# Kernel tuning notes

Hardware: AMD Instinct MI355X
Metric: run time of the kernel (lower is better)

Reference implementation:

```python
import jax, jax.numpy as jnp
import numpy as np

# dims: batch B, frames F_, spatial tokens N, heads H, head dim D, model dim DIM
B, F_, N, H, D, DIM = 1, 16, 1024, 8, 64, 512


def setup_inputs() -> dict:
    key = jax.random.key(0)
    k1, k2, k3, k4 = jax.random.split(key, 4)
    x = jax.random.normal(k1, (B, F_ * N, DIM), dtype=jnp.float32)
    W_qkv = jax.random.normal(k2, (DIM, 3 * H * D), dtype=jnp.float32) * 0.02
    W_out = jax.random.normal(k3, (H * D, DIM), dtype=jnp.float32) * 0.02
    mask = jax.random.randint(k4, (1, 1, N), 0, 2, dtype=jnp.int32)
    return {"x": x, "W_qkv": W_qkv, "W_out": W_out, "mask": mask, "diag": 1}


def reference(x, W_qkv, W_out, mask, diag):
    scale = D ** -0.5
    qkv = x @ W_qkv                      # [B, F*N, 3*H*D]
    q, k, v = jnp.split(qkv, 3, axis=-1)

    def split_heads(t):                  # 'b n (h d) -> (b h) n d'
        return t.reshape(B, F_ * N, H, D).transpose(0, 2, 1, 3).reshape(B * H, F_ * N, D)

    q, k, v = map(split_heads, (q, k, v))
    q = q * scale

    def axial(t):                        # '(b h) (f n) d -> (b h f) n d'
        return t.reshape(B * H * F_, N, D)

    q, k, v = map(axial, (q, k, v))

    sim = jnp.einsum('bid,bjd->bij', q, k)        # [(B*H*F), N, N]
    neg = -jnp.finfo(sim.dtype).max
    if diag:
        sim = jnp.where(jnp.eye(N, dtype=bool)[None], neg, sim)
    sim = jnp.where(mask == 0, neg, sim)           # padding mask broadcast
    attn = jax.nn.softmax(sim, axis=-1)
    out = jnp.einsum('bij,bjd->bid', attn, v)      # [(B*H*F), N, D]

    # '(b h f) n d -> (b h) (f n) d' then '(b h) n d -> b n (h d)'
    out = out.reshape(B, H, F_ * N, D).transpose(0, 2, 1, 3).reshape(B, F_ * N, H * D)
    return out @ W_out
```

## Files before the change

kernel.cpp:

```cpp
#include <hip/hip_runtime.h>
#include <stdint.h>

typedef __bf16 bf16;
typedef __bf16 bf16x8 __attribute__((ext_vector_type(8)));
typedef float f32x4 __attribute__((ext_vector_type(4)));

__device__ __forceinline__ void gload_lds16(const void* g, void* l) {
    __builtin_amdgcn_global_load_lds((const __attribute__((address_space(1))) void*)g,
                                     (__attribute__((address_space(3))) void*)l, 16, 0, 0);
}

__device__ __forceinline__ float fast_exp2(float x) { return __builtin_amdgcn_exp2f(x); }

__global__ __launch_bounds__(256) void k_cvt(const float* __restrict__ x, bf16* __restrict__ xb, int n8) {
    int i = blockIdx.x * 256 + threadIdx.x;
    if (i >= n8) return;
    const f32x4* p = (const f32x4*)(x + (size_t)i * 8);
    f32x4 a = p[0], b = p[1];
    bf16x8 o;
    o[0] = (bf16)a[0]; o[1] = (bf16)a[1]; o[2] = (bf16)a[2]; o[3] = (bf16)a[3];
    o[4] = (bf16)b[0]; o[5] = (bf16)b[1]; o[6] = (bf16)b[2]; o[7] = (bf16)b[3];
    *(bf16x8*)(xb + (size_t)i * 8) = o;
}

__global__ __launch_bounds__(256) void k_tx(const float* __restrict__ W, bf16* __restrict__ WT, int R, int C) {
    __shared__ float t[32][33];
    int n0 = blockIdx.x * 32, k0 = blockIdx.y * 32;
    int tx = threadIdx.x, ty = threadIdx.y;
    for (int i = 0; i < 32; i += 8) t[ty + i][tx] = W[(size_t)(k0 + ty + i) * C + n0 + tx];
    __syncthreads();
    for (int i = 0; i < 32; i += 8) WT[(size_t)(n0 + ty + i) * R + k0 + tx] = (bf16)t[tx][ty + i];
}

__global__ __launch_bounds__(256) void k_scan(const int* __restrict__ mask, int* __restrict__ idxU,
                                              int* __restrict__ cpos, int* __restrict__ meta) {
    __shared__ int lsum[256];
    int t = threadIdx.x;
    int m[4], s = 0;
#pragma unroll
    for (int e = 0; e < 4; e++) { m[e] = mask[4 * t + e]; s += m[e]; }
    lsum[t] = s;
    __syncthreads();
    for (int off = 1; off < 256; off <<= 1) {
        int v = (t >= off) ? lsum[t - off] : 0;
        __syncthreads();
        lsum[t] += v;
        __syncthreads();
    }
    int run = lsum[t] - s;
#pragma unroll
    for (int e = 0; e < 4; e++) {
        if (m[e]) { idxU[run] = 4 * t + e; cpos[4 * t + e] = run; run++; }
        else cpos[4 * t + e] = -1;
    }
    if (t == 255) { meta[0] = lsum[255]; meta[1] = (lsum[255] + 63) >> 6; }
}

__global__ __launch_bounds__(256) void k_zpad(bf16* __restrict__ Kc, const int* __restrict__ meta) {
    int bp = blockIdx.x;
    int nU = meta[0], nUp = meta[1] << 6;
    int n = (nUp - nU) * 64;
    for (int idx = threadIdx.x; idx < n; idx += 256) {
        int r = nU + (idx >> 6), d = idx & 63;
        Kc[((size_t)bp * 1024 + r) * 64 + d] = (bf16)0.f;
    }
}

__global__ __launch_bounds__(512) void k_qkv(const bf16* __restrict__ Xb, const bf16* __restrict__ WT,
                                             bf16* __restrict__ Qb, bf16* __restrict__ Kc,
                                             bf16* __restrict__ Vc, const int* __restrict__ cpos) {
    __shared__ char As[32768], Bs[16384];
    int tid = threadIdx.x, l = tid & 63, w = tid >> 6;
    int wy = w & 3, wx = w >> 2;
    int id = blockIdx.x;
    int wg = (id & 7) * 96 + (id >> 3);
    int bm = (wg / 12) * 256, bn = (wg % 12) * 128;
    int lr = l & 15, kg = l >> 4;
    int rsub = tid >> 3;
    int csrc = (tid & 7) ^ (rsub & 7);
    f32x4 acc[4][4] = {};

    for (int k0 = 0; k0 < 512; k0 += 64) {
        __syncthreads();
#pragma unroll
        for (int i = 0; i < 4; i++)
            gload_lds16((const char*)Xb + ((size_t)(bm + i * 64 + rsub) * 512 + k0) * 2 + csrc * 16,
                        As + i * 8192 + tid * 16);
#pragma unroll
        for (int i = 0; i < 2; i++)
            gload_lds16((const char*)WT + ((size_t)(bn + i * 64 + rsub) * 512 + k0) * 2 + csrc * 16,
                        Bs + i * 8192 + tid * 16);
        __syncthreads();
#pragma unroll
        for (int kk = 0; kk < 2; kk++) {
            int sb = kk * 4 + kg;
            bf16x8 af[4], bfr[4];
#pragma unroll
            for (int mt = 0; mt < 4; mt++) {
                int r = wy * 64 + mt * 16 + lr;
                af[mt] = *(const bf16x8*)(As + r * 128 + ((sb ^ (r & 7)) << 4));
            }
#pragma unroll
            for (int nt = 0; nt < 4; nt++) {
                int r = wx * 64 + nt * 16 + lr;
                bfr[nt] = *(const bf16x8*)(Bs + r * 128 + ((sb ^ (r & 7)) << 4));
            }
#pragma unroll
            for (int mt = 0; mt < 4; mt++)
#pragma unroll
                for (int nt = 0; nt < 4; nt++)
                    acc[mt][nt] = __builtin_amdgcn_mfma_f32_16x16x32_bf16(af[mt], bfr[nt], acc[mt][nt], 0, 0, 0);
        }
    }

    int cb = bn + wx * 64;
    int which = cb >> 9, hd = cb & 511, h = hd >> 6;
#pragma unroll
    for (int mt = 0; mt < 4; mt++) {
#pragma unroll
        for (int j = 0; j < 4; j++) {
            int m = bm + wy * 64 + mt * 16 + kg * 4 + j;
            int f = m >> 10, nn = m & 1023;
            int bpb = h * 16 + f;
            if (which == 0) {
#pragma unroll
                for (int nt = 0; nt < 4; nt++)
                    Qb[((size_t)bpb * 1024 + nn) * 64 + nt * 16 + lr] = (bf16)(acc[mt][nt][j] * 0.18033688f);
            } else {
                int cr = cpos[nn];
                if (cr >= 0) {
                    bf16* base = (which == 1) ? Kc : Vc;
#pragma unroll
                    for (int nt = 0; nt < 4; nt++)
                        base[((size_t)bpb * 1024 + cr) * 64 + nt * 16 + lr] = (bf16)acc[mt][nt][j];
                }
            }
        }
    }
}

__global__ __launch_bounds__(256) void k_vtg(const bf16* __restrict__ Vc, bf16* __restrict__ Vtc,
                                             const int* __restrict__ meta) {
    __shared__ bf16 t[64][80];
    int bp = blockIdx.y, c0 = blockIdx.x * 64;
    int nU = meta[0], nUp = meta[1] << 6;
    if (c0 >= nUp) return;
    int tid = threadIdx.x;
    int nl = tid >> 2, dc = (tid & 3) * 16;
    int c = c0 + nl;
    bf16x8 a0 = {}, a1 = {};
    if (c < nU) {
        const bf16* src = Vc + ((size_t)bp * 1024 + c) * 64 + dc;
        a0 = *(const bf16x8*)src;
        a1 = *(const bf16x8*)(src + 8);
    }
    *(bf16x8*)&t[nl][dc] = a0;
    *(bf16x8*)&t[nl][dc + 8] = a1;
    __syncthreads();
    int dl = tid >> 2, nc = (tid & 3) * 16;
    bf16x8 o0, o1;
#pragma unroll
    for (int i = 0; i < 8; i++) o0[i] = t[nc + i][dl];
#pragma unroll
    for (int i = 0; i < 8; i++) o1[i] = t[nc + 8 + i][dl];
    bf16* dst = Vtc + ((size_t)bp * 64 + dl) * 1024 + c0 + nc;
    *(bf16x8*)dst = o0;
    *(bf16x8*)(dst + 8) = o1;
}

__global__ __launch_bounds__(512) void k_attn(const bf16* __restrict__ Qb, const bf16* __restrict__ Kc,
                                              const bf16* __restrict__ Vtc, bf16* __restrict__ AO,
                                              const int* __restrict__ cpos, const int* __restrict__ meta,
                                              const int* __restrict__ diagp) {
    __shared__ char Ks[8192], Vs[8192], Ps[16384];
    int tid = threadIdx.x, l = tid & 63, w = tid >> 6;
    int id = blockIdx.x;
    int wg = (id & 7) * 128 + (id >> 3);
    int qt = wg & 7, bp = wg >> 3;
    int lr = l & 15, kg = l >> 4;
    int diag = diagp[0];
    int nU = meta[0], nT = meta[1];

    int nq = qt * 128 + w * 16 + lr;
    const char* Qrow = (const char*)Qb + ((size_t)bp * 1024 + nq) * 128;
    bf16x8 qf0 = *(const bf16x8*)(Qrow + kg * 16);
    bf16x8 qf1 = *(const bf16x8*)(Qrow + 64 + kg * 16);

    int cq[4];
#pragma unroll
    for (int j = 0; j < 4; j++) {
        int qg = qt * 128 + w * 16 + kg * 4 + j;
        cq[j] = diag ? cpos[qg] : -1;
    }

    const char* Kbase = (const char*)Kc + (size_t)bp * 1024 * 128;
    const char* Vbase = (const char*)Vtc + (size_t)bp * 64 * 2048;

    int rs = tid >> 3;
    int cs = (tid & 7) ^ (rs & 7);

    f32x4 o[4] = {};
    f32x4 psum = {0.f, 0.f, 0.f, 0.f};

    for (int kt = 0; kt < nT; kt++) {
        __syncthreads();
        gload_lds16(Kbase + (size_t)(kt * 64 + rs) * 128 + cs * 16, Ks + w * 1024);
        gload_lds16(Vbase + (size_t)rs * 2048 + kt * 128 + cs * 16, Vs + w * 1024);
        __syncthreads();

        f32x4 s[4] = {};
#pragma unroll
        for (int nt = 0; nt < 4; nt++) {
            int r = nt * 16 + lr;
            bf16x8 kf0 = *(const bf16x8*)(Ks + r * 128 + ((kg ^ (r & 7)) << 4));
            bf16x8 kf1 = *(const bf16x8*)(Ks + r * 128 + (((4 + kg) ^ (r & 7)) << 4));
            s[nt] = __builtin_amdgcn_mfma_f32_16x16x32_bf16(qf0, kf0, s[nt], 0, 0, 0);
            s[nt] = __builtin_amdgcn_mfma_f32_16x16x32_bf16(qf1, kf1, s[nt], 0, 0, 0);
        }

        float mf0 = (kt * 64 + lr < nU) ? 1.f : 0.f;
        float mf1 = (kt * 64 + 16 + lr < nU) ? 1.f : 0.f;
        float mf2 = (kt * 64 + 32 + lr < nU) ? 1.f : 0.f;
        float mf3 = (kt * 64 + 48 + lr < nU) ? 1.f : 0.f;
#pragma unroll
        for (int j = 0; j < 4; j++) {
            s[0][j] = fast_exp2(s[0][j]) * mf0;
            s[1][j] = fast_exp2(s[1][j]) * mf1;
            s[2][j] = fast_exp2(s[2][j]) * mf2;
            s[3][j] = fast_exp2(s[3][j]) * mf3;
        }
#pragma unroll
        for (int nt = 0; nt < 4; nt++) {
            int c = kt * 64 + nt * 16 + lr;
#pragma unroll
            for (int j = 0; j < 4; j++)
                if (c == cq[j]) s[nt][j] = 0.f;
        }
#pragma unroll
        for (int j = 0; j < 4; j++) psum[j] += (s[0][j] + s[1][j]) + (s[2][j] + s[3][j]);

#pragma unroll
        for (int nt = 0; nt < 4; nt++)
#pragma unroll
            for (int j = 0; j < 4; j++) {
                int rq = w * 16 + kg * 4 + j;
                int byte = (rq * 128 + (nt * 16 + lr) * 2) ^ ((rq & 7) << 4);
                *(bf16*)(Ps + byte) = (bf16)s[nt][j];
            }

        int rp = w * 16 + lr;
        bf16x8 pf0 = *(const bf16x8*)(Ps + rp * 128 + ((kg ^ (rp & 7)) << 4));
        bf16x8 pf1 = *(const bf16x8*)(Ps + rp * 128 + (((4 + kg) ^ (rp & 7)) << 4));
#pragma unroll
        for (int dt = 0; dt < 4; dt++) {
            int rd = dt * 16 + lr;
            bf16x8 vf0 = *(const bf16x8*)(Vs + rd * 128 + ((kg ^ (rd & 7)) << 4));
            bf16x8 vf1 = *(const bf16x8*)(Vs + rd * 128 + (((4 + kg) ^ (rd & 7)) << 4));
            o[dt] = __builtin_amdgcn_mfma_f32_16x16x32_bf16(pf0, vf0, o[dt], 0, 0, 0);
            o[dt] = __builtin_amdgcn_mfma_f32_16x16x32_bf16(pf1, vf1, o[dt], 0, 0, 0);
        }
    }

#pragma unroll
    for (int off = 1; off < 16; off <<= 1)
#pragma unroll
        for (int j = 0; j < 4; j++) psum[j] += __shfl_xor(psum[j], off, 64);
    float inv[4];
#pragma unroll
    for (int j = 0; j < 4; j++) inv[j] = 1.0f / psum[j];

    int f = bp & 15, h = bp >> 4;
#pragma unroll
    for (int dt = 0; dt < 4; dt++)
#pragma unroll
        for (int j = 0; j < 4; j++) {
            int n = qt * 128 + w * 16 + kg * 4 + j;
            size_t m = (size_t)f * 1024 + n;
            AO[m * 512 + h * 64 + dt * 16 + lr] = (bf16)(o[dt][j] * inv[j]);
        }
}

__global__ __launch_bounds__(256) void k_out(const bf16* __restrict__ Ab, const bf16* __restrict__ WT,
                                             float* __restrict__ out) {
    __shared__ char As[16384], Bs[16384];
    int tid = threadIdx.x, l = tid & 63, w = tid >> 6;
    int wy = w >> 1, wx = w & 1;
    int id = blockIdx.x;
    int wg = (id & 7) * 64 + (id >> 3);
    int bm = (wg / 4) * 128, bn = (wg % 4) * 128;
    int lr = l & 15, kg = l >> 4;
    int p = l & 7, rsub = l >> 3;
    int csrc = p ^ rsub;
    f32x4 acc[4][4] = {};

    for (int k0 = 0; k0 < 512; k0 += 64) {
        __syncthreads();
#pragma unroll
        for (int i = 0; i < 4; i++) {
            int rt = w * 32 + i * 8 + rsub;
            gload_lds16((const char*)Ab + ((size_t)(bm + rt) * 512 + k0) * 2 + csrc * 16,
                        As + w * 4096 + i * 1024 + l * 16);
            gload_lds16((const char*)WT + ((size_t)(bn + rt) * 512 + k0) * 2 + csrc * 16,
                        Bs + w * 4096 + i * 1024 + l * 16);
        }
        __syncthreads();
#pragma unroll
        for (int kk = 0; kk < 2; kk++) {
            bf16x8 af[4], bfr[4];
            int sb = (kk * 4 + kg);
#pragma unroll
            for (int mt = 0; mt < 4; mt++) {
                int r = wy * 64 + mt * 16 + lr;
                af[mt] = *(const bf16x8*)(As + r * 128 + ((sb ^ (lr & 7)) << 4));
            }
#pragma unroll
            for (int nt = 0; nt < 4; nt++) {
                int r = wx * 64 + nt * 16 + lr;
                bfr[nt] = *(const bf16x8*)(Bs + r * 128 + ((sb ^ (lr & 7)) << 4));
            }
#pragma unroll
            for (int mt = 0; mt < 4; mt++)
#pragma unroll
                for (int nt = 0; nt < 4; nt++)
                    acc[mt][nt] = __builtin_amdgcn_mfma_f32_16x16x32_bf16(af[mt], bfr[nt], acc[mt][nt], 0, 0, 0);
        }
    }
#pragma unroll
    for (int mt = 0; mt < 4; mt++)
#pragma unroll
        for (int nt = 0; nt < 4; nt++) {
            int c = bn + wx * 64 + nt * 16 + lr;
#pragma unroll
            for (int j = 0; j < 4; j++) {
                int m = bm + wy * 64 + mt * 16 + kg * 4 + j;
                out[(size_t)m * 512 + c] = acc[mt][nt][j];
            }
        }
}

extern "C" void kernel_launch(void* const* d_in, const int* in_sizes, int n_in,
                              void* d_out, int out_size, void* d_ws, size_t ws_size,
                              hipStream_t stream) {
    const float* x    = (const float*)d_in[0];
    const float* Wqkv = (const float*)d_in[1];
    const float* Wout = (const float*)d_in[2];
    const int*   mask = (const int*)d_in[3];
    const int*   diag = (const int*)d_in[4];
    float* out = (float*)d_out;
    char* ws = (char*)d_ws;

    bf16* Xb  = (bf16*)(ws);
    bf16* AO  = (bf16*)(ws);
    bf16* WqT = (bf16*)(ws + ((size_t)16 << 20));
    bf16* WoT = (bf16*)(ws + ((size_t)18 << 20));
    int*  idxU = (int*)(ws + ((size_t)18 << 20) + (1 << 19));
    int*  cpos = (int*)(ws + ((size_t)18 << 20) + (1 << 19) + 4096);
    int*  meta = (int*)(ws + ((size_t)18 << 20) + (1 << 19) + 8192);
    bf16* Qb  = (bf16*)(ws + ((size_t)19 << 20));
    bf16* Kc  = (bf16*)(ws + ((size_t)35 << 20));
    bf16* Vc  = (bf16*)(ws + ((size_t)51 << 20));
    bf16* Vtc = (bf16*)(ws + ((size_t)67 << 20));

    hipLaunchKernelGGL(k_cvt, dim3(4096), dim3(256), 0, stream, x, Xb, 1048576);
    hipLaunchKernelGGL(k_tx,  dim3(48, 16), dim3(32, 8), 0, stream, Wqkv, WqT, 512, 1536);
    hipLaunchKernelGGL(k_tx,  dim3(16, 16), dim3(32, 8), 0, stream, Wout, WoT, 512, 512);
    hipLaunchKernelGGL(k_scan, dim3(1), dim3(256), 0, stream, mask, idxU, cpos, meta);
    hipLaunchKernelGGL(k_zpad, dim3(128), dim3(256), 0, stream, Kc, meta);
    hipLaunchKernelGGL(k_qkv, dim3(768), dim3(512), 0, stream, Xb, WqT, Qb, Kc, Vc, cpos);
    hipLaunchKernelGGL(k_vtg, dim3(16, 128), dim3(256), 0, stream, Vc, Vtc, meta);
    hipLaunchKernelGGL(k_attn, dim3(1024), dim3(512), 0, stream, Qb, Kc, Vtc, AO, cpos, meta, diag);
    hipLaunchKernelGGL(k_out, dim3(512), dim3(256), 0, stream, AO, WoT, out);
}
```

Measured before the change: 123.0 us.

## Shrink QKV GEMM tile to 128x128 and load two KV tiles per attention sync

The QKV projection kernel goes from 512-thread blocks with 256x128 tiles to 256-thread blocks with 128x128 tiles. The grid doubles to 1536 blocks, LDS per block shrinks, and the load swizzle is rewritten per wave. The attention kernel now double-buffers K/V in LDS, loading two 64-key tiles between one pair of barriers so the barrier count per key is halved. This trades more LDS per attention block, and possibly lower occupancy, for fewer synchronisations, and trades A-tile reuse in the GEMM for more parallel blocks.

```diff
diff --git a/kernel.cpp b/kernel.cpp
--- a/kernel.cpp
+++ b/kernel.cpp
@@ -66,44 +66,44 @@
     }
 }
 
-__global__ __launch_bounds__(512) void k_qkv(const bf16* __restrict__ Xb, const bf16* __restrict__ WT,
+__global__ __launch_bounds__(256) void k_qkv(const bf16* __restrict__ Xb, const bf16* __restrict__ WT,
                                              bf16* __restrict__ Qb, bf16* __restrict__ Kc,
                                              bf16* __restrict__ Vc, const int* __restrict__ cpos) {
-    __shared__ char As[32768], Bs[16384];
+    __shared__ char As[16384], Bs[16384];
     int tid = threadIdx.x, l = tid & 63, w = tid >> 6;
-    int wy = w & 3, wx = w >> 2;
+    int wy = w >> 1, wx = w & 1;
     int id = blockIdx.x;
-    int wg = (id & 7) * 96 + (id >> 3);
-    int bm = (wg / 12) * 256, bn = (wg % 12) * 128;
+    int wg = (id & 7) * 192 + (id >> 3);
+    int bm = (wg / 12) * 128, bn = (wg % 12) * 128;
     int lr = l & 15, kg = l >> 4;
-    int rsub = tid >> 3;
-    int csrc = (tid & 7) ^ (rsub & 7);
+    int p = l & 7, rsub = l >> 3;
+    int csrc = p ^ rsub;
     f32x4 acc[4][4] = {};
 
     for (int k0 = 0; k0 < 512; k0 += 64) {
         __syncthreads();
 #pragma unroll
-        for (int i = 0; i < 4; i++)
-            gload_lds16((const char*)Xb + ((size_t)(bm + i * 64 + rsub) * 512 + k0) * 2 + csrc * 16,
-                        As + i * 8192 + tid * 16);
-#pragma unroll
-        for (int i = 0; i < 2; i++)
-            gload_lds16((const char*)WT + ((size_t)(bn + i * 64 + rsub) * 512 + k0) * 2 + csrc * 16,
-                        Bs + i * 8192 + tid * 16);
+        for (int i = 0; i < 4; i++) {
+            int rt = w * 32 + i * 8 + rsub;
+            gload_lds16((const char*)Xb + ((size_t)(bm + rt) * 512 + k0) * 2 + csrc * 16,
+                        As + w * 4096 + i * 1024 + l * 16);
+            gload_lds16((const char*)WT + ((size_t)(bn + rt) * 512 + k0) * 2 + csrc * 16,
+                        Bs + w * 4096 + i * 1024 + l * 16);
+        }
         __syncthreads();
 #pragma unroll
         for (int kk = 0; kk < 2; kk++) {
-            int sb = kk * 4 + kg;
             bf16x8 af[4], bfr[4];
+            int sb = (kk * 4 + kg);
 #pragma unroll
             for (int mt = 0; mt < 4; mt++) {
                 int r = wy * 64 + mt * 16 + lr;
-                af[mt] = *(const bf16x8*)(As + r * 128 + ((sb ^ (r & 7)) << 4));
+                af[mt] = *(const bf16x8*)(As + r * 128 + ((sb ^ (lr & 7)) << 4));
             }
 #pragma unroll
             for (int nt = 0; nt < 4; nt++) {
                 int r = wx * 64 + nt * 16 + lr;
-                bfr[nt] = *(const bf16x8*)(Bs + r * 128 + ((sb ^ (r & 7)) << 4));
+                bfr[nt] = *(const bf16x8*)(Bs + r * 128 + ((sb ^ (lr & 7)) << 4));
             }
 #pragma unroll
             for (int mt = 0; mt < 4; mt++)
@@ -172,7 +172,7 @@
                                               const bf16* __restrict__ Vtc, bf16* __restrict__ AO,
                                               const int* __restrict__ cpos, const int* __restrict__ meta,
                                               const int* __restrict__ diagp) {
-    __shared__ char Ks[8192], Vs[8192], Ps[16384];
+    __shared__ char Ks[2][8192], Vs[2][8192], Ps[16384];
     int tid = threadIdx.x, l = tid & 63, w = tid >> 6;
     int id = blockIdx.x;
     int wg = (id & 7) * 128 + (id >> 3);
@@ -180,6 +180,7 @@
     int lr = l & 15, kg = l >> 4;
     int diag = diagp[0];
     int nU = meta[0], nT = meta[1];
+    int nT2 = (nT + 1) >> 1;
 
     int nq = qt * 128 + w * 16 + lr;
     const char* Qrow = (const char*)Qb + ((size_t)bp * 1024 + nq) * 128;
@@ -202,62 +203,74 @@
     f32x4 o[4] = {};
     f32x4 psum = {0.f, 0.f, 0.f, 0.f};
 
-    for (int kt = 0; kt < nT; kt++) {
-        __syncthreads();
-        gload_lds16(Kbase + (size_t)(kt * 64 + rs) * 128 + cs * 16, Ks + w * 1024);
-        gload_lds16(Vbase + (size_t)rs * 2048 + kt * 128 + cs * 16, Vs + w * 1024);
-        __syncthreads();
-
-        f32x4 s[4] = {};
-#pragma unroll
-        for (int nt = 0; nt < 4; nt++) {
-            int r = nt * 16 + lr;
-            bf16x8 kf0 = *(const bf16x8*)(Ks + r * 128 + ((kg ^ (r & 7)) << 4));
-            bf16x8 kf1 = *(const bf16x8*)(Ks + r * 128 + (((4 + kg) ^ (r & 7)) << 4));
-            s[nt] = __builtin_amdgcn_mfma_f32_16x16x32_bf16(qf0, kf0, s[nt], 0, 0, 0);
-            s[nt] = __builtin_amdgcn_mfma_f32_16x16x32_bf16(qf1, kf1, s[nt], 0, 0, 0);
-        }
-
-        float mf0 = (kt * 64 + lr < nU) ? 1.f : 0.f;
-        float mf1 = (kt * 64 + 16 + lr < nU) ? 1.f : 0.f;
-        float mf2 = (kt * 64 + 32 + lr < nU) ? 1.f : 0.f;
-        float mf3 = (kt * 64 + 48 + lr < nU) ? 1.f : 0.f;
-#pragma unroll
-        for (int j = 0; j < 4; j++) {
-            s[0][j] = fast_exp2(s[0][j]) * mf0;
-            s[1][j] = fast_exp2(s[1][j]) * mf1;
-            s[2][j] = fast_exp2(s[2][j]) * mf2;
-            s[3][j] = fast_exp2(s[3][j]) * mf3;
-        }
-#pragma unroll
-        for (int nt = 0; nt < 4; nt++) {
-            int c = kt * 64 + nt * 16 + lr;
-#pragma unroll
-            for (int j = 0; j < 4; j++)
-                if (c == cq[j]) s[nt][j] = 0.f;
-        }
-#pragma unroll
-        for (int j = 0; j < 4; j++) psum[j] += (s[0][j] + s[1][j]) + (s[2][j] + s[3][j]);
-
-#pragma unroll
-        for (int nt = 0; nt < 4; nt++)
+    for (int kt2 = 0; kt2 < nT2; kt2++) {
+        int ktA = kt2 * 2;
+        int nH = (ktA + 1 < nT) ? 2 : 1;
+        __syncthreads();
+        gload_lds16(Kbase + (size_t)(ktA * 64 + rs) * 128 + cs * 16, Ks[0] + w * 1024);
+        gload_lds16(Vbase + (size_t)rs * 2048 + ktA * 128 + cs * 16, Vs[0] + w * 1024);
+        if (nH == 2) {
+            gload_lds16(Kbase + (size_t)((ktA + 1) * 64 + rs) * 128 + cs * 16, Ks[1] + w * 1024);
+            gload_lds16(Vbase + (size_t)rs * 2048 + (ktA + 1) * 128 + cs * 16, Vs[1] + w * 1024);
+        }
+        __syncthreads();
+
+        for (int hh = 0; hh < nH; hh++) {
+            int kt = ktA + hh;
+            const char* Kt = Ks[hh];
+            const char* Vt = Vs[hh];
+
+            f32x4 s[4] = {};
+#pragma unroll
+            for (int nt = 0; nt < 4; nt++) {
+                int r = nt * 16 + lr;
+                bf16x8 kf0 = *(const bf16x8*)(Kt + r * 128 + ((kg ^ (r & 7)) << 4));
+                bf16x8 kf1 = *(const bf16x8*)(Kt + r * 128 + (((4 + kg) ^ (r & 7)) << 4));
+                s[nt] = __builtin_amdgcn_mfma_f32_16x16x32_bf16(qf0, kf0, s[nt], 0, 0, 0);
+                s[nt] = __builtin_amdgcn_mfma_f32_16x16x32_bf16(qf1, kf1, s[nt], 0, 0, 0);
+            }
+
+            float mf0 = (kt * 64 + lr < nU) ? 1.f : 0.f;
+            float mf1 = (kt * 64 + 16 + lr < nU) ? 1.f : 0.f;
+            float mf2 = (kt * 64 + 32 + lr < nU) ? 1.f : 0.f;
+            float mf3 = (kt * 64 + 48 + lr < nU) ? 1.f : 0.f;
 #pragma unroll
             for (int j = 0; j < 4; j++) {
-                int rq = w * 16 + kg * 4 + j;
-                int byte = (rq * 128 + (nt * 16 + lr) * 2) ^ ((rq & 7) << 4);
-                *(bf16*)(Ps + byte) = (bf16)s[nt][j];
-            }
-
-        int rp = w * 16 + lr;
-        bf16x8 pf0 = *(const bf16x8*)(Ps + rp * 128 + ((kg ^ (rp & 7)) << 4));
-        bf16x8 pf1 = *(const bf16x8*)(Ps + rp * 128 + (((4 + kg) ^ (rp & 7)) << 4));
-#pragma unroll
-        for (int dt = 0; dt < 4; dt++) {
-            int rd = dt * 16 + lr;
-            bf16x8 vf0 = *(const bf16x8*)(Vs + rd * 128 + ((kg ^ (rd & 7)) << 4));
-            bf16x8 vf1 = *(const bf16x8*)(Vs + rd * 128 + (((4 + kg) ^ (rd & 7)) << 4));
-            o[dt] = __builtin_amdgcn_mfma_f32_16x16x32_bf16(pf0, vf0, o[dt], 0, 0, 0);
-            o[dt] = __builtin_amdgcn_mfma_f32_16x16x32_bf16(pf1, vf1, o[dt], 0, 0, 0);
+                s[0][j] = fast_exp2(s[0][j]) * mf0;
+                s[1][j] = fast_exp2(s[1][j]) * mf1;
+                s[2][j] = fast_exp2(s[2][j]) * mf2;
+                s[3][j] = fast_exp2(s[3][j]) * mf3;
+            }
+#pragma unroll
+            for (int nt = 0; nt < 4; nt++) {
+                int c = kt * 64 + nt * 16 + lr;
+#pragma unroll
+                for (int j = 0; j < 4; j++)
+                    if (c == cq[j]) s[nt][j] = 0.f;
+            }
+#pragma unroll
+            for (int j = 0; j < 4; j++) psum[j] += (s[0][j] + s[1][j]) + (s[2][j] + s[3][j]);
+
+#pragma unroll
+            for (int nt = 0; nt < 4; nt++)
+#pragma unroll
+                for (int j = 0; j < 4; j++) {
+                    int rq = w * 16 + kg * 4 + j;
+                    int byte = (rq * 128 + (nt * 16 + lr) * 2) ^ ((rq & 7) << 4);
+                    *(bf16*)(Ps + byte) = (bf16)s[nt][j];
+                }
+
+            int rp = w * 16 + lr;
+            bf16x8 pf0 = *(const bf16x8*)(Ps + rp * 128 + ((kg ^ (rp & 7)) << 4));
+            bf16x8 pf1 = *(const bf16x8*)(Ps + rp * 128 + (((4 + kg) ^ (rp & 7)) << 4));
+#pragma unroll
+            for (int dt = 0; dt < 4; dt++) {
+                int rd = dt * 16 + lr;
+                bf16x8 vf0 = *(const bf16x8*)(Vt + rd * 128 + ((kg ^ (rd & 7)) << 4));
+                bf16x8 vf1 = *(const bf16x8*)(Vt + rd * 128 + (((4 + kg) ^ (rd & 7)) << 4));
+                o[dt] = __builtin_amdgcn_mfma_f32_16x16x32_bf16(pf0, vf0, o[dt], 0, 0, 0);
+                o[dt] = __builtin_amdgcn_mfma_f32_16x16x32_bf16(pf1, vf1, o[dt], 0, 0, 0);
+            }
         }
     }
 
@@ -366,7 +379,7 @@
     hipLaunchKernelGGL(k_tx,  dim3(16, 16), dim3(32, 8), 0, stream, Wout, WoT, 512, 512);
     hipLaunchKernelGGL(k_scan, dim3(1), dim3(256), 0, stream, mask, idxU, cpos, meta);
     hipLaunchKernelGGL(k_zpad, dim3(128), dim3(256), 0, stream, Kc, meta);
-    hipLaunchKernelGGL(k_qkv, dim3(768), dim3(512), 0, stream, Xb, WqT, Qb, Kc, Vc, cpos);
+    hipLaunchKernelGGL(k_qkv, dim3(1536), dim3(256), 0, stream, Xb, WqT, Qb, Kc, Vc, cpos);
     hipLaunchKernelGGL(k_vtg, dim3(16, 128), dim3(256), 0, stream, Vc, Vtc, meta);
     hipLaunchKernelGGL(k_attn, dim3(1024), dim3(512), 0, stream, Qb, Kc, Vtc, AO, cpos, meta, diag);
     hipLaunchKernelGGL(k_out, dim3(512), dim3(256), 0, stream, AO, WoT, out);
```

New measurement: 136.6 us. 11.1% more time.
